# Performance work log

Hardware: AMD Instinct MI355X
Metric: run time of the kernel (lower is better)

The kernel has to match this reference:

```python
import jax, jax.numpy as jnp
import numpy as np
from jax import lax

H = 64
IN = 3

def _lstm_layer(x, Wih, Whh, bih, bhh, collect):
    # x: [B, T, in]; Wih: [4H, in]; Whh: [4H, H]. PyTorch gate order: i, f, g, o.
    B = x.shape[0]
    h0 = jnp.zeros((B, H), x.dtype)
    c0 = jnp.zeros((B, H), x.dtype)
    b = bih + bhh
    def step(carry, xt):
        h, c = carry
        gates = xt @ Wih.T + h @ Whh.T + b  # [B, 4H]
        i, f, g, o = jnp.split(gates, 4, axis=-1)
        i = jax.nn.sigmoid(i); f = jax.nn.sigmoid(f)
        g = jnp.tanh(g); o = jax.nn.sigmoid(o)
        c = f * c + i * g
        h = o * jnp.tanh(c)
        return (h, c), (h if collect else None)
    xs = jnp.swapaxes(x, 0, 1)  # [T, B, in]
    (h, c), hs = lax.scan(step, (h0, c0), xs)
    if collect:
        return jnp.swapaxes(hs, 0, 1)  # [B, T, H]
    return h  # [B, H]


def setup_inputs() -> dict:
    key = jax.random.key(0)
    ks = jax.random.split(key, 14)
    s = 1.0 / np.sqrt(H)
    def u(k, shape):
        return jax.random.uniform(k, shape, jnp.float32, -s, s)
    return {
        "x": jax.random.normal(ks[0], (4096, 512, IN), jnp.float32),
        "Wih0": u(ks[1], (4 * H, IN)), "Whh0": u(ks[2], (4 * H, H)),
        "bih0": u(ks[3], (4 * H,)), "bhh0": u(ks[4], (4 * H,)),
        "Wih1": u(ks[5], (4 * H, H)), "Whh1": u(ks[6], (4 * H, H)),
        "bih1": u(ks[7], (4 * H,)), "bhh1": u(ks[8], (4 * H,)),
        "Wc1": jax.random.normal(ks[9], (32, H), jnp.float32) * 0.1,
        "bc1": jnp.zeros((32,), jnp.float32),
        "Wc2": jax.random.normal(ks[10], (1, 32), jnp.float32) * 0.1,
        "bc2": jnp.zeros((1,), jnp.float32),
    }


def reference(x, Wih0, Whh0, bih0, bhh0, Wih1, Whh1, bih1, bhh1, Wc1, bc1, Wc2, bc2):
    # 2-layer LSTM (dropout inactive at inference); only last timestep of layer 2 is used.
    h1 = _lstm_layer(x, Wih0, Whh0, bih0, bhh0, collect=True)   # [B, T, H]
    last = _lstm_layer(h1, Wih1, Whh1, bih1, bhh1, collect=False)  # [B, H]
    hidden = jax.nn.relu(last @ Wc1.T + bc1)  # [B, 32]
    out = jax.nn.sigmoid(hidden @ Wc2.T + bc2)  # [B, 1]
    return out
```

## Files before the change

### kernel.cpp

```cpp
#include <hip/hip_runtime.h>

#define TSEQ   512
#define BATCH  4096
#define MROWS  16

typedef short bf16x8 __attribute__((ext_vector_type(8)));
typedef short bf16x4 __attribute__((ext_vector_type(4)));
typedef float f32x4  __attribute__((ext_vector_type(4)));
typedef float f32x2  __attribute__((ext_vector_type(2)));

#define NL2E  (-1.44269504f)
#define P2L2E (2.88539008f)

__device__ __forceinline__ unsigned short f2bf(float f) {
    unsigned int u = __builtin_bit_cast(unsigned int, f);
    return (unsigned short)((u + 0x8000u) >> 16);
}

__device__ __forceinline__ f32x2 cellupd2(const f32x4 a, const f32x4 b, f32x2& C) {
    f32x2 ei = {__builtin_amdgcn_exp2f(a[0]), __builtin_amdgcn_exp2f(b[0])};
    f32x2 ef = {__builtin_amdgcn_exp2f(a[1]), __builtin_amdgcn_exp2f(b[1])};
    f32x2 eg = {__builtin_amdgcn_exp2f(a[2]), __builtin_amdgcn_exp2f(b[2])};
    f32x2 eo = {__builtin_amdgcn_exp2f(a[3]), __builtin_amdgcn_exp2f(b[3])};
    f32x2 A  = 1.f + ei;
    f32x2 G1 = eg + 1.f;
    f32x2 F  = 1.f + ef;
    f32x2 t  = A * G1;
    f32x2 G2 = eg * P2L2E + (NL2E * 2.f);
    f32x2 num = C * t + G2 * F;
    f32x2 den = t * F;
    f32x2 r  = {__builtin_amdgcn_rcpf(den.x), __builtin_amdgcn_rcpf(den.y)};
    f32x2 Cn = num * r;
    Cn.x = fminf(Cn.x, 126.f);
    Cn.y = fminf(Cn.y, 126.f);
    C = Cn;
    f32x2 ec = {__builtin_amdgcn_exp2f(Cn.x), __builtin_amdgcn_exp2f(Cn.y)};
    f32x2 B  = 1.f + eo;
    f32x2 hn = ec - 1.f;
    f32x2 hd = B * (ec + 1.f);
    f32x2 rr = {__builtin_amdgcn_rcpf(hd.x), __builtin_amdgcn_rcpf(hd.y)};
    return hn * rr;
}


__global__ __launch_bounds__(1024, 4) void lstm2_kernel(
    const float* __restrict__ x,
    const float* __restrict__ Wih0, const float* __restrict__ Whh0,
    const float* __restrict__ bih0, const float* __restrict__ bhh0,
    const float* __restrict__ Wih1, const float* __restrict__ Whh1,
    const float* __restrict__ bih1, const float* __restrict__ bhh1,
    const float* __restrict__ Wc1,  const float* __restrict__ bc1,
    const float* __restrict__ Wc2,  const float* __restrict__ bc2,
    float* __restrict__ out)
{
    __shared__ __align__(16) unsigned short ring[2][MROWS * 64];
    __shared__ __align__(16) unsigned short h2s[2][MROWS * 64];
    __shared__ __align__(16) unsigned short xq[64][128];
    __shared__ float h2f[MROWS][65];
    __shared__ float hid[MROWS][33];

    const int tid  = threadIdx.x;
    const int wv   = tid >> 6;
    const int lane = tid & 63;
    const int col  = lane & 15;
    const int lg   = lane >> 4;
    const int b0   = blockIdx.x * MROWS;
    const int sw   = (col & 7) << 4;

    ((unsigned int*)ring)[tid] = 0u;
    ((unsigned int*)h2s)[tid]  = 0u;

    const int xrow = (tid >> 5) & 15;
    const int xt   = tid & 31;
    const float* xb = x + ((size_t)(b0 + xrow) * TSEQ + xt) * 3;
    float xr0 = 0.f, xr1 = 0.f, xr2 = 0.f;
    if (tid < 512) {
        xr0 = xb[0]; xr1 = xb[1]; xr2 = xb[2];
        bf16x8 xf = {(short)f2bf(xr0),(short)f2bf(xr1),(short)f2bf(xr2),0,0,0,0,0};
        *(bf16x8*)((char*)xq + (xt << 8) + ((xrow << 4) ^ ((xt & 7) << 4))) = xf;
        xr0 = xb[96]; xr1 = xb[97]; xr2 = xb[98];
    }
    __syncthreads();

    const int rd0 = (col * 128 +      lg * 16) ^ sw;
    const int rd1 = (col * 128 + 64 + lg * 16) ^ sw;

#define FLUSH(S) do { \
    if (((S) & 31) == 16 && (S) < 480) { \
        const int c1_ = ((S) >> 5) + 1; \
        const int t64_ = ((c1_ & 1) << 5) + xt; \
        bf16x8 xf_ = {(short)f2bf(xr0),(short)f2bf(xr1),(short)f2bf(xr2),0,0,0,0,0}; \
        *(bf16x8*)((char*)xq + (t64_ << 8) + ((xrow << 4) ^ ((xt & 7) << 4))) = xf_; \
        if (c1_ < 15) { const float* p_ = xb + (c1_ + 1) * 96; xr0 = p_[0]; xr1 = p_[1]; xr2 = p_[2]; } \
    } \
} while(0)

    if (wv < 8) {
        const int wq = wv;
        const int ga = col & 3;
        const float sca = (ga == 2) ? P2L2E : NL2E;
        bf16x8 Wf[2][3];
        f32x4 bia4[2];
#pragma unroll
        for (int tt = 0; tt < 2; ++tt) {
            const int n = ga * 64 + 16 * (col >> 2) + 2 * wq + tt;
#pragma unroll
            for (int f = 0; f < 3; ++f)
#pragma unroll
                for (int i = 0; i < 8; ++i) {
                    const int k = f * 32 + lg * 8 + i;
                    float v = 0.f;
                    if (k < 64)      v = Whh0[n * 64 + k];
                    else if (k < 67) v = Wih0[n * 3 + (k - 64)];
                    Wf[tt][f][i] = (short)f2bf(sca * v);
                }
#pragma unroll
            for (int r = 0; r < 4; ++r) {
                const int nb = r * 64 + 16 * lg + 2 * wq + tt;
                bia4[tt][r] = ((r == 2) ? P2L2E : NL2E) * (bih0[nb] + bhh0[nb]);
            }
        }
        const int hw = (col * 128 + 32 * lg + 4 * wq) ^ sw;
        f32x2 C01 = {0.f, 0.f};

#define L1B(RI, WI, S) do { \
        const char* rb_ = (const char*)ring[RI]; \
        bf16x8 v0_ = *(const bf16x8*)(rb_ + rd0); \
        bf16x8 v1_ = *(const bf16x8*)(rb_ + rd1); \
        bf16x8 v2_ = {0,0,0,0,0,0,0,0}; \
        if (lg == 0) \
            v2_ = *(const bf16x8*)((const char*)xq + ((((S)&63)) << 8) + ((col << 4) ^ (((S)&7) << 4))); \
        f32x4 a0_ = __builtin_amdgcn_mfma_f32_16x16x32_bf16(Wf[0][0], v0_, bia4[0],0,0,0); \
        f32x4 a1_ = __builtin_amdgcn_mfma_f32_16x16x32_bf16(Wf[1][0], v0_, bia4[1],0,0,0); \
        a0_ = __builtin_amdgcn_mfma_f32_16x16x32_bf16(Wf[0][1], v1_, a0_,0,0,0); \
        a1_ = __builtin_amdgcn_mfma_f32_16x16x32_bf16(Wf[1][1], v1_, a1_,0,0,0); \
        a0_ = __builtin_amdgcn_mfma_f32_16x16x32_bf16(Wf[0][2], v2_, a0_,0,0,0); \
        a1_ = __builtin_amdgcn_mfma_f32_16x16x32_bf16(Wf[1][2], v2_, a1_,0,0,0); \
        f32x2 h01_ = cellupd2(a0_, a1_, C01); \
        unsigned int p0_; \
        asm("v_cvt_pk_bf16_f32 %0, %1, %2" : "=v"(p0_) : "v"(h01_.x), "v"(h01_.y)); \
        *(unsigned int*)((char*)ring[WI] + hw) = p0_; \
    } while(0)

        L1B(1, 0, 0);
        __syncthreads();
#pragma unroll 1
        for (int m = 0; m < 255; ++m) {
            const int s1 = 2 * m + 1;
            L1B(0, 1, s1);
            __syncthreads();
            L1B(1, 0, s1 + 1);
            FLUSH(s1 + 1);
            __syncthreads();
        }
        L1B(0, 1, 511);
        __syncthreads();
        __syncthreads();
#undef L1B
    } else {
        const int wq = wv - 8;
        const int ga = col & 3;
        const float sca = (ga == 2) ? P2L2E : NL2E;
        bf16x8 Wf[2][4];
        f32x4 bia4[2];
#pragma unroll
        for (int tt = 0; tt < 2; ++tt) {
            const int n = ga * 64 + 16 * (col >> 2) + 2 * wq + tt;
#pragma unroll
            for (int f = 0; f < 4; ++f)
#pragma unroll
                for (int i = 0; i < 8; ++i) {
                    const int k = f * 32 + lg * 8 + i;
                    const float v = (k < 64) ? Wih1[n * 64 + k] : Whh1[n * 64 + (k - 64)];
                    Wf[tt][f][i] = (short)f2bf(sca * v);
                }
#pragma unroll
            for (int r = 0; r < 4; ++r) {
                const int nb = r * 64 + 16 * lg + 2 * wq + tt;
                bia4[tt][r] = ((r == 2) ? P2L2E : NL2E) * (bih1[nb] + bhh1[nb]);
            }
        }
        const int hw2 = (col * 128 + 32 * lg + 4 * wq) ^ sw;
        f32x2 C01 = {0.f, 0.f};
        f32x2 hv01 = {0.f, 0.f};

#define L2B(RB, HR) do { \
        const char* rb_ = (const char*)ring[RB]; \
        const char* hp_ = (const char*)h2s[HR]; \
        bf16x8 v0_ = *(const bf16x8*)(rb_ + rd0); \
        bf16x8 v1_ = *(const bf16x8*)(rb_ + rd1); \
        bf16x8 v2_ = *(const bf16x8*)(hp_ + rd0); \
        bf16x8 v3_ = *(const bf16x8*)(hp_ + rd1); \
        f32x4 a0_ = __builtin_amdgcn_mfma_f32_16x16x32_bf16(Wf[0][0], v0_, bia4[0],0,0,0); \
        f32x4 a1_ = __builtin_amdgcn_mfma_f32_16x16x32_bf16(Wf[1][0], v0_, bia4[1],0,0,0); \
        a0_ = __builtin_amdgcn_mfma_f32_16x16x32_bf16(Wf[0][1], v1_, a0_,0,0,0); \
        a1_ = __builtin_amdgcn_mfma_f32_16x16x32_bf16(Wf[1][1], v1_, a1_,0,0,0); \
        a0_ = __builtin_amdgcn_mfma_f32_16x16x32_bf16(Wf[0][2], v2_, a0_,0,0,0); \
        a1_ = __builtin_amdgcn_mfma_f32_16x16x32_bf16(Wf[1][2], v2_, a1_,0,0,0); \
        a0_ = __builtin_amdgcn_mfma_f32_16x16x32_bf16(Wf[0][3], v3_, a0_,0,0,0); \
        a1_ = __builtin_amdgcn_mfma_f32_16x16x32_bf16(Wf[1][3], v3_, a1_,0,0,0); \
        hv01 = cellupd2(a0_, a1_, C01); \
        unsigned int p0_; \
        asm("v_cvt_pk_bf16_f32 %0, %1, %2" : "=v"(p0_) : "v"(hv01.x), "v"(hv01.y)); \
        *(unsigned int*)((char*)h2s[RB] + hw2) = p0_; \
    } while(0)

        __syncthreads();
#pragma unroll 1
        for (int m = 0; m < 255; ++m) {
            L2B(0, 1);
            __syncthreads();
            L2B(1, 0);
            __syncthreads();
        }
        L2B(0, 1);
        __syncthreads();
        L2B(1, 0);
        __syncthreads();
#undef L2B
        const int ub = 16 * lg + 2 * wq;
        h2f[col][ub + 0] = hv01.x;
        h2f[col][ub + 1] = hv01.y;
    }
    __syncthreads();

    if (tid < 512) {
        const int b = tid & 15, j = tid >> 4;
        float s = bc1[j];
#pragma unroll 8
        for (int k = 0; k < 64; ++k) s += Wc1[j * 64 + k] * h2f[b][k];
        hid[b][j] = fmaxf(s, 0.f);
    }
    __syncthreads();
    if (tid < 16) {
        float s = bc2[0];
#pragma unroll 8
        for (int k = 0; k < 32; ++k) s += Wc2[k] * hid[tid][k];
        float e = __builtin_amdgcn_exp2f(NL2E * s);
        out[b0 + tid] = __builtin_amdgcn_rcpf(1.f + e);
    }
}

extern "C" void kernel_launch(void* const* d_in, const int* in_sizes, int n_in,
                              void* d_out, int out_size, void* d_ws, size_t ws_size,
                              hipStream_t stream) {
    lstm2_kernel<<<BATCH / MROWS, 1024, 0, stream>>>(
        (const float*)d_in[0],
        (const float*)d_in[1], (const float*)d_in[2],
        (const float*)d_in[3], (const float*)d_in[4],
        (const float*)d_in[5], (const float*)d_in[6],
        (const float*)d_in[7], (const float*)d_in[8],
        (const float*)d_in[9], (const float*)d_in[10],
        (const float*)d_in[11], (const float*)d_in[12],
        (float*)d_out);
}
```

Measured before the change: 293.3 us.

## Software-pipeline LDS operand loads across LSTM layer barriers with one-step lag

```diff
diff --git a/kernel.cpp b/kernel.cpp
--- a/kernel.cpp
+++ b/kernel.cpp
@@ -5,7 +5,6 @@
 #define MROWS  16
 
 typedef short bf16x8 __attribute__((ext_vector_type(8)));
-typedef short bf16x4 __attribute__((ext_vector_type(4)));
 typedef float f32x4  __attribute__((ext_vector_type(4)));
 typedef float f32x2  __attribute__((ext_vector_type(2)));
 
@@ -95,6 +94,8 @@
     } \
 } while(0)
 
+#define XQRD(S) (*(const bf16x8*)((const char*)xq + ((((S)&63)) << 8) + ((col << 4) ^ (((S)&7) << 4))))
+
     if (wv < 8) {
         const int wq = wv;
         const int ga = col & 3;
@@ -122,20 +123,19 @@
         }
         const int hw = (col * 128 + 32 * lg + 4 * wq) ^ sw;
         f32x2 C01 = {0.f, 0.f};
+        bf16x8 pv2 = XQRD(0);
 
 #define L1B(RI, WI, S) do { \
         const char* rb_ = (const char*)ring[RI]; \
         bf16x8 v0_ = *(const bf16x8*)(rb_ + rd0); \
         bf16x8 v1_ = *(const bf16x8*)(rb_ + rd1); \
-        bf16x8 v2_ = {0,0,0,0,0,0,0,0}; \
-        if (lg == 0) \
-            v2_ = *(const bf16x8*)((const char*)xq + ((((S)&63)) << 8) + ((col << 4) ^ (((S)&7) << 4))); \
-        f32x4 a0_ = __builtin_amdgcn_mfma_f32_16x16x32_bf16(Wf[0][0], v0_, bia4[0],0,0,0); \
-        f32x4 a1_ = __builtin_amdgcn_mfma_f32_16x16x32_bf16(Wf[1][0], v0_, bia4[1],0,0,0); \
+        f32x4 a0_ = __builtin_amdgcn_mfma_f32_16x16x32_bf16(Wf[0][2], pv2, bia4[0],0,0,0); \
+        f32x4 a1_ = __builtin_amdgcn_mfma_f32_16x16x32_bf16(Wf[1][2], pv2, bia4[1],0,0,0); \
+        a0_ = __builtin_amdgcn_mfma_f32_16x16x32_bf16(Wf[0][0], v0_, a0_,0,0,0); \
+        a1_ = __builtin_amdgcn_mfma_f32_16x16x32_bf16(Wf[1][0], v0_, a1_,0,0,0); \
         a0_ = __builtin_amdgcn_mfma_f32_16x16x32_bf16(Wf[0][1], v1_, a0_,0,0,0); \
         a1_ = __builtin_amdgcn_mfma_f32_16x16x32_bf16(Wf[1][1], v1_, a1_,0,0,0); \
-        a0_ = __builtin_amdgcn_mfma_f32_16x16x32_bf16(Wf[0][2], v2_, a0_,0,0,0); \
-        a1_ = __builtin_amdgcn_mfma_f32_16x16x32_bf16(Wf[1][2], v2_, a1_,0,0,0); \
+        pv2 = XQRD((S) + 1); \
         f32x2 h01_ = cellupd2(a0_, a1_, C01); \
         unsigned int p0_; \
         asm("v_cvt_pk_bf16_f32 %0, %1, %2" : "=v"(p0_) : "v"(h01_.x), "v"(h01_.y)); \
@@ -149,11 +149,12 @@
             const int s1 = 2 * m + 1;
             L1B(0, 1, s1);
             __syncthreads();
+            FLUSH(s1 + 1);
             L1B(1, 0, s1 + 1);
-            FLUSH(s1 + 1);
             __syncthreads();
         }
         L1B(0, 1, 511);
+        __syncthreads();
         __syncthreads();
         __syncthreads();
 #undef L1B
@@ -183,18 +184,23 @@
         const int hw2 = (col * 128 + 32 * lg + 4 * wq) ^ sw;
         f32x2 C01 = {0.f, 0.f};
         f32x2 hv01 = {0.f, 0.f};
-
-#define L2B(RB, HR) do { \
-        const char* rb_ = (const char*)ring[RB]; \
-        const char* hp_ = (const char*)h2s[HR]; \
-        bf16x8 v0_ = *(const bf16x8*)(rb_ + rd0); \
-        bf16x8 v1_ = *(const bf16x8*)(rb_ + rd1); \
+        bf16x8 pv0, pv1;
+
+#define PF(P) do { \
+        const char* pb_ = (const char*)ring[P]; \
+        pv0 = *(const bf16x8*)(pb_ + rd0); \
+        pv1 = *(const bf16x8*)(pb_ + rd1); \
+    } while(0)
+
+#define L2B(WB, PFC) do { \
+        const char* hp_ = (const char*)h2s[(WB) ^ 1]; \
         bf16x8 v2_ = *(const bf16x8*)(hp_ + rd0); \
         bf16x8 v3_ = *(const bf16x8*)(hp_ + rd1); \
-        f32x4 a0_ = __builtin_amdgcn_mfma_f32_16x16x32_bf16(Wf[0][0], v0_, bia4[0],0,0,0); \
-        f32x4 a1_ = __builtin_amdgcn_mfma_f32_16x16x32_bf16(Wf[1][0], v0_, bia4[1],0,0,0); \
-        a0_ = __builtin_amdgcn_mfma_f32_16x16x32_bf16(Wf[0][1], v1_, a0_,0,0,0); \
-        a1_ = __builtin_amdgcn_mfma_f32_16x16x32_bf16(Wf[1][1], v1_, a1_,0,0,0); \
+        f32x4 a0_ = __builtin_amdgcn_mfma_f32_16x16x32_bf16(Wf[0][0], pv0, bia4[0],0,0,0); \
+        f32x4 a1_ = __builtin_amdgcn_mfma_f32_16x16x32_bf16(Wf[1][0], pv0, bia4[1],0,0,0); \
+        a0_ = __builtin_amdgcn_mfma_f32_16x16x32_bf16(Wf[0][1], pv1, a0_,0,0,0); \
+        a1_ = __builtin_amdgcn_mfma_f32_16x16x32_bf16(Wf[1][1], pv1, a1_,0,0,0); \
+        PFC; \
         a0_ = __builtin_amdgcn_mfma_f32_16x16x32_bf16(Wf[0][2], v2_, a0_,0,0,0); \
         a1_ = __builtin_amdgcn_mfma_f32_16x16x32_bf16(Wf[1][2], v2_, a1_,0,0,0); \
         a0_ = __builtin_amdgcn_mfma_f32_16x16x32_bf16(Wf[0][3], v3_, a0_,0,0,0); \
@@ -202,22 +208,25 @@
         hv01 = cellupd2(a0_, a1_, C01); \
         unsigned int p0_; \
         asm("v_cvt_pk_bf16_f32 %0, %1, %2" : "=v"(p0_) : "v"(hv01.x), "v"(hv01.y)); \
-        *(unsigned int*)((char*)h2s[RB] + hw2) = p0_; \
+        *(unsigned int*)((char*)h2s[WB] + hw2) = p0_; \
     } while(0)
 
+        __syncthreads();
+        PF(0);
         __syncthreads();
 #pragma unroll 1
         for (int m = 0; m < 255; ++m) {
-            L2B(0, 1);
-            __syncthreads();
-            L2B(1, 0);
-            __syncthreads();
-        }
-        L2B(0, 1);
-        __syncthreads();
-        L2B(1, 0);
+            L2B(0, PF(1));
+            __syncthreads();
+            L2B(1, PF(0));
+            __syncthreads();
+        }
+        L2B(0, PF(1));
+        __syncthreads();
+        L2B(1, (void)0);
         __syncthreads();
 #undef L2B
+#undef PF
         const int ub = 16 * lg + 2 * wq;
         h2f[col][ub + 0] = hv01.x;
         h2f[col][ub + 1] = hv01.y;
```

New measurement: 299.4 us. +2.1%, slower.

## Merge both LSTM layers into each wave, halving block size

Applied to the files above, without the earlier changes.

```diff
diff --git a/kernel.cpp b/kernel.cpp
--- a/kernel.cpp
+++ b/kernel.cpp
@@ -5,7 +5,6 @@
 #define MROWS  16
 
 typedef short bf16x8 __attribute__((ext_vector_type(8)));
-typedef short bf16x4 __attribute__((ext_vector_type(4)));
 typedef float f32x4  __attribute__((ext_vector_type(4)));
 typedef float f32x2  __attribute__((ext_vector_type(2)));
 
@@ -43,7 +42,7 @@
 }
 
 
-__global__ __launch_bounds__(1024, 4) void lstm2_kernel(
+__global__ __launch_bounds__(512, 2) void lstm2_kernel(
     const float* __restrict__ x,
     const float* __restrict__ Wih0, const float* __restrict__ Whh0,
     const float* __restrict__ bih0, const float* __restrict__ bhh0,
@@ -67,19 +66,20 @@
     const int b0   = blockIdx.x * MROWS;
     const int sw   = (col & 7) << 4;
 
-    ((unsigned int*)ring)[tid] = 0u;
-    ((unsigned int*)h2s)[tid]  = 0u;
-
-    const int xrow = (tid >> 5) & 15;
+    for (int i = tid; i < 1024; i += 512) {
+        ((unsigned int*)ring)[i] = 0u;
+        ((unsigned int*)h2s)[i]  = 0u;
+    }
+
+    const int xrow = tid >> 5;
     const int xt   = tid & 31;
     const float* xb = x + ((size_t)(b0 + xrow) * TSEQ + xt) * 3;
-    float xr0 = 0.f, xr1 = 0.f, xr2 = 0.f;
-    if (tid < 512) {
-        xr0 = xb[0]; xr1 = xb[1]; xr2 = xb[2];
+    float xr0 = xb[0], xr1 = xb[1], xr2 = xb[2];
+    {
         bf16x8 xf = {(short)f2bf(xr0),(short)f2bf(xr1),(short)f2bf(xr2),0,0,0,0,0};
         *(bf16x8*)((char*)xq + (xt << 8) + ((xrow << 4) ^ ((xt & 7) << 4))) = xf;
-        xr0 = xb[96]; xr1 = xb[97]; xr2 = xb[98];
-    }
+    }
+    xr0 = xb[96]; xr1 = xb[97]; xr2 = xb[98];
     __syncthreads();
 
     const int rd0 = (col * 128 +      lg * 16) ^ sw;
@@ -95,136 +95,142 @@
     } \
 } while(0)
 
-    if (wv < 8) {
-        const int wq = wv;
-        const int ga = col & 3;
-        const float sca = (ga == 2) ? P2L2E : NL2E;
-        bf16x8 Wf[2][3];
-        f32x4 bia4[2];
-#pragma unroll
-        for (int tt = 0; tt < 2; ++tt) {
-            const int n = ga * 64 + 16 * (col >> 2) + 2 * wq + tt;
-#pragma unroll
-            for (int f = 0; f < 3; ++f)
-#pragma unroll
-                for (int i = 0; i < 8; ++i) {
-                    const int k = f * 32 + lg * 8 + i;
-                    float v = 0.f;
-                    if (k < 64)      v = Whh0[n * 64 + k];
-                    else if (k < 67) v = Wih0[n * 3 + (k - 64)];
-                    Wf[tt][f][i] = (short)f2bf(sca * v);
-                }
-#pragma unroll
-            for (int r = 0; r < 4; ++r) {
-                const int nb = r * 64 + 16 * lg + 2 * wq + tt;
-                bia4[tt][r] = ((r == 2) ? P2L2E : NL2E) * (bih0[nb] + bhh0[nb]);
+#define XQRD(S) (*(const bf16x8*)((const char*)xq + ((((S)&63)) << 8) + ((col << 4) ^ (((S)&7) << 4))))
+#define MM(A,B,C) __builtin_amdgcn_mfma_f32_16x16x32_bf16((A),(B),(C),0,0,0)
+
+    const int wq = wv;
+    const int ga = col & 3;
+    const float sca = (ga == 2) ? P2L2E : NL2E;
+    bf16x8 WfL1[2][3];
+    f32x4 biaL1[2];
+#pragma unroll
+    for (int tt = 0; tt < 2; ++tt) {
+        const int n = ga * 64 + 16 * (col >> 2) + 2 * wq + tt;
+#pragma unroll
+        for (int f = 0; f < 3; ++f)
+#pragma unroll
+            for (int i = 0; i < 8; ++i) {
+                const int k = f * 32 + lg * 8 + i;
+                float v = 0.f;
+                if (k < 64)      v = Whh0[n * 64 + k];
+                else if (k < 67) v = Wih0[n * 3 + (k - 64)];
+                WfL1[tt][f][i] = (short)f2bf(sca * v);
             }
+#pragma unroll
+        for (int r = 0; r < 4; ++r) {
+            const int nb = r * 64 + 16 * lg + 2 * wq + tt;
+            biaL1[tt][r] = ((r == 2) ? P2L2E : NL2E) * (bih0[nb] + bhh0[nb]);
         }
-        const int hw = (col * 128 + 32 * lg + 4 * wq) ^ sw;
-        f32x2 C01 = {0.f, 0.f};
-
-#define L1B(RI, WI, S) do { \
-        const char* rb_ = (const char*)ring[RI]; \
-        bf16x8 v0_ = *(const bf16x8*)(rb_ + rd0); \
-        bf16x8 v1_ = *(const bf16x8*)(rb_ + rd1); \
-        bf16x8 v2_ = {0,0,0,0,0,0,0,0}; \
-        if (lg == 0) \
-            v2_ = *(const bf16x8*)((const char*)xq + ((((S)&63)) << 8) + ((col << 4) ^ (((S)&7) << 4))); \
-        f32x4 a0_ = __builtin_amdgcn_mfma_f32_16x16x32_bf16(Wf[0][0], v0_, bia4[0],0,0,0); \
-        f32x4 a1_ = __builtin_amdgcn_mfma_f32_16x16x32_bf16(Wf[1][0], v0_, bia4[1],0,0,0); \
-        a0_ = __builtin_amdgcn_mfma_f32_16x16x32_bf16(Wf[0][1], v1_, a0_,0,0,0); \
-        a1_ = __builtin_amdgcn_mfma_f32_16x16x32_bf16(Wf[1][1], v1_, a1_,0,0,0); \
-        a0_ = __builtin_amdgcn_mfma_f32_16x16x32_bf16(Wf[0][2], v2_, a0_,0,0,0); \
-        a1_ = __builtin_amdgcn_mfma_f32_16x16x32_bf16(Wf[1][2], v2_, a1_,0,0,0); \
-        f32x2 h01_ = cellupd2(a0_, a1_, C01); \
-        unsigned int p0_; \
-        asm("v_cvt_pk_bf16_f32 %0, %1, %2" : "=v"(p0_) : "v"(h01_.x), "v"(h01_.y)); \
-        *(unsigned int*)((char*)ring[WI] + hw) = p0_; \
-    } while(0)
-
-        L1B(1, 0, 0);
-        __syncthreads();
-#pragma unroll 1
-        for (int m = 0; m < 255; ++m) {
-            const int s1 = 2 * m + 1;
-            L1B(0, 1, s1);
-            __syncthreads();
-            L1B(1, 0, s1 + 1);
-            FLUSH(s1 + 1);
-            __syncthreads();
+    }
+    bf16x8 WfL2[2][4];
+    f32x4 biaL2[2];
+#pragma unroll
+    for (int tt = 0; tt < 2; ++tt) {
+        const int n = ga * 64 + 16 * (col >> 2) + 2 * wq + tt;
+#pragma unroll
+        for (int f = 0; f < 4; ++f)
+#pragma unroll
+            for (int i = 0; i < 8; ++i) {
+                const int k = f * 32 + lg * 8 + i;
+                const float v = (k < 64) ? Wih1[n * 64 + k] : Whh1[n * 64 + (k - 64)];
+                WfL2[tt][f][i] = (short)f2bf(sca * v);
+            }
+#pragma unroll
+        for (int r = 0; r < 4; ++r) {
+            const int nb = r * 64 + 16 * lg + 2 * wq + tt;
+            biaL2[tt][r] = ((r == 2) ? P2L2E : NL2E) * (bih1[nb] + bhh1[nb]);
         }
-        L1B(0, 1, 511);
-        __syncthreads();
-        __syncthreads();
-#undef L1B
-    } else {
-        const int wq = wv - 8;
-        const int ga = col & 3;
-        const float sca = (ga == 2) ? P2L2E : NL2E;
-        bf16x8 Wf[2][4];
-        f32x4 bia4[2];
-#pragma unroll
-        for (int tt = 0; tt < 2; ++tt) {
-            const int n = ga * 64 + 16 * (col >> 2) + 2 * wq + tt;
-#pragma unroll
-            for (int f = 0; f < 4; ++f)
-#pragma unroll
-                for (int i = 0; i < 8; ++i) {
-                    const int k = f * 32 + lg * 8 + i;
-                    const float v = (k < 64) ? Wih1[n * 64 + k] : Whh1[n * 64 + (k - 64)];
-                    Wf[tt][f][i] = (short)f2bf(sca * v);
-                }
-#pragma unroll
-            for (int r = 0; r < 4; ++r) {
-                const int nb = r * 64 + 16 * lg + 2 * wq + tt;
-                bia4[tt][r] = ((r == 2) ? P2L2E : NL2E) * (bih1[nb] + bhh1[nb]);
-            }
-        }
-        const int hw2 = (col * 128 + 32 * lg + 4 * wq) ^ sw;
-        f32x2 C01 = {0.f, 0.f};
-        f32x2 hv01 = {0.f, 0.f};
-
-#define L2B(RB, HR) do { \
-        const char* rb_ = (const char*)ring[RB]; \
-        const char* hp_ = (const char*)h2s[HR]; \
+    }
+    const int hw = (col * 128 + 32 * lg + 4 * wq) ^ sw;
+    f32x2 C_L1 = {0.f, 0.f};
+    f32x2 C_L2 = {0.f, 0.f};
+    f32x2 hv01 = {0.f, 0.f};
+    bf16x8 pv2 = XQRD(0);
+
+#define MRG(P, S) do { \
+        const char* rb_ = (const char*)ring[P]; \
+        const char* hp_ = (const char*)h2s[(P) ^ 1]; \
         bf16x8 v0_ = *(const bf16x8*)(rb_ + rd0); \
         bf16x8 v1_ = *(const bf16x8*)(rb_ + rd1); \
         bf16x8 v2_ = *(const bf16x8*)(hp_ + rd0); \
         bf16x8 v3_ = *(const bf16x8*)(hp_ + rd1); \
-        f32x4 a0_ = __builtin_amdgcn_mfma_f32_16x16x32_bf16(Wf[0][0], v0_, bia4[0],0,0,0); \
-        f32x4 a1_ = __builtin_amdgcn_mfma_f32_16x16x32_bf16(Wf[1][0], v0_, bia4[1],0,0,0); \
-        a0_ = __builtin_amdgcn_mfma_f32_16x16x32_bf16(Wf[0][1], v1_, a0_,0,0,0); \
-        a1_ = __builtin_amdgcn_mfma_f32_16x16x32_bf16(Wf[1][1], v1_, a1_,0,0,0); \
-        a0_ = __builtin_amdgcn_mfma_f32_16x16x32_bf16(Wf[0][2], v2_, a0_,0,0,0); \
-        a1_ = __builtin_amdgcn_mfma_f32_16x16x32_bf16(Wf[1][2], v2_, a1_,0,0,0); \
-        a0_ = __builtin_amdgcn_mfma_f32_16x16x32_bf16(Wf[0][3], v3_, a0_,0,0,0); \
-        a1_ = __builtin_amdgcn_mfma_f32_16x16x32_bf16(Wf[1][3], v3_, a1_,0,0,0); \
-        hv01 = cellupd2(a0_, a1_, C01); \
+        f32x4 b0_ = MM(WfL1[0][2], pv2, biaL1[0]); \
+        f32x4 b1_ = MM(WfL1[1][2], pv2, biaL1[1]); \
+        b0_ = MM(WfL1[0][0], v0_, b0_); \
+        b1_ = MM(WfL1[1][0], v0_, b1_); \
+        f32x4 c0_ = MM(WfL2[0][0], v0_, biaL2[0]); \
+        f32x4 c1_ = MM(WfL2[1][0], v0_, biaL2[1]); \
+        b0_ = MM(WfL1[0][1], v1_, b0_); \
+        b1_ = MM(WfL1[1][1], v1_, b1_); \
+        pv2 = XQRD((S) + 1); \
+        f32x2 hL1_ = cellupd2(b0_, b1_, C_L1); \
+        c0_ = MM(WfL2[0][1], v1_, c0_); \
+        c1_ = MM(WfL2[1][1], v1_, c1_); \
+        c0_ = MM(WfL2[0][2], v2_, c0_); \
+        c1_ = MM(WfL2[1][2], v2_, c1_); \
+        c0_ = MM(WfL2[0][3], v3_, c0_); \
+        c1_ = MM(WfL2[1][3], v3_, c1_); \
         unsigned int p0_; \
-        asm("v_cvt_pk_bf16_f32 %0, %1, %2" : "=v"(p0_) : "v"(hv01.x), "v"(hv01.y)); \
-        *(unsigned int*)((char*)h2s[RB] + hw2) = p0_; \
+        asm("v_cvt_pk_bf16_f32 %0, %1, %2" : "=v"(p0_) : "v"(hL1_.x), "v"(hL1_.y)); \
+        *(unsigned int*)((char*)ring[(P) ^ 1] + hw) = p0_; \
+        hv01 = cellupd2(c0_, c1_, C_L2); \
+        unsigned int p1_; \
+        asm("v_cvt_pk_bf16_f32 %0, %1, %2" : "=v"(p1_) : "v"(hv01.x), "v"(hv01.y)); \
+        *(unsigned int*)((char*)h2s[P] + hw) = p1_; \
     } while(0)
 
+    {
+        const char* rb_ = (const char*)ring[1];
+        bf16x8 v0_ = *(const bf16x8*)(rb_ + rd0);
+        bf16x8 v1_ = *(const bf16x8*)(rb_ + rd1);
+        f32x4 b0_ = MM(WfL1[0][2], pv2, biaL1[0]);
+        f32x4 b1_ = MM(WfL1[1][2], pv2, biaL1[1]);
+        b0_ = MM(WfL1[0][0], v0_, b0_);
+        b1_ = MM(WfL1[1][0], v0_, b1_);
+        b0_ = MM(WfL1[0][1], v1_, b0_);
+        b1_ = MM(WfL1[1][1], v1_, b1_);
+        pv2 = XQRD(1);
+        f32x2 hL1_ = cellupd2(b0_, b1_, C_L1);
+        unsigned int p0_;
+        asm("v_cvt_pk_bf16_f32 %0, %1, %2" : "=v"(p0_) : "v"(hL1_.x), "v"(hL1_.y));
+        *(unsigned int*)((char*)ring[0] + hw) = p0_;
+    }
+    __syncthreads();
+
+#pragma unroll 1
+    for (int m = 0; m < 255; ++m) {
+        MRG(0, 2 * m + 1);
         __syncthreads();
-#pragma unroll 1
-        for (int m = 0; m < 255; ++m) {
-            L2B(0, 1);
-            __syncthreads();
-            L2B(1, 0);
-            __syncthreads();
-        }
-        L2B(0, 1);
+        FLUSH(2 * m + 2);
+        MRG(1, 2 * m + 2);
         __syncthreads();
-        L2B(1, 0);
-        __syncthreads();
-#undef L2B
-        const int ub = 16 * lg + 2 * wq;
-        h2f[col][ub + 0] = hv01.x;
-        h2f[col][ub + 1] = hv01.y;
-    }
-    __syncthreads();
-
-    if (tid < 512) {
+    }
+    MRG(0, 511);
+    __syncthreads();
+
+    {
+        const char* rb_ = (const char*)ring[1];
+        const char* hp_ = (const char*)h2s[0];
+        bf16x8 v0_ = *(const bf16x8*)(rb_ + rd0);
+        bf16x8 v1_ = *(const bf16x8*)(rb_ + rd1);
+        bf16x8 v2_ = *(const bf16x8*)(hp_ + rd0);
+        bf16x8 v3_ = *(const bf16x8*)(hp_ + rd1);
+        f32x4 c0_ = MM(WfL2[0][0], v0_, biaL2[0]);
+        f32x4 c1_ = MM(WfL2[1][0], v0_, biaL2[1]);
+        c0_ = MM(WfL2[0][1], v1_, c0_);
+        c1_ = MM(WfL2[1][1], v1_, c1_);
+        c0_ = MM(WfL2[0][2], v2_, c0_);
+        c1_ = MM(WfL2[1][2], v2_, c1_);
+        c0_ = MM(WfL2[0][3], v3_, c0_);
+        c1_ = MM(WfL2[1][3], v3_, c1_);
+        hv01 = cellupd2(c0_, c1_, C_L2);
+    }
+    const int ub = 16 * lg + 2 * wq;
+    h2f[col][ub + 0] = hv01.x;
+    h2f[col][ub + 1] = hv01.y;
+    __syncthreads();
+
+    {
         const int b = tid & 15, j = tid >> 4;
         float s = bc1[j];
 #pragma unroll 8
@@ -244,7 +250,7 @@
 extern "C" void kernel_launch(void* const* d_in, const int* in_sizes, int n_in,
                               void* d_out, int out_size, void* d_ws, size_t ws_size,
                               hipStream_t stream) {
-    lstm2_kernel<<<BATCH / MROWS, 1024, 0, stream>>>(
+    lstm2_kernel<<<BATCH / MROWS, 512, 0, stream>>>(
         (const float*)d_in[0],
         (const float*)d_in[1], (const float*)d_in[2],
         (const float*)d_in[3], (const float*)d_in[4],
```

New measurement: 326.4 us. 11.3% more time.

## Halve batch rows per block, use 512-thread blocks with swizzled MFMA outputs

Applied to the files above, without the earlier changes.

```diff
diff --git a/kernel.cpp b/kernel.cpp
--- a/kernel.cpp
+++ b/kernel.cpp
@@ -2,10 +2,9 @@
 
 #define TSEQ   512
 #define BATCH  4096
-#define MROWS  16
+#define MROWS  8
 
 typedef short bf16x8 __attribute__((ext_vector_type(8)));
-typedef short bf16x4 __attribute__((ext_vector_type(4)));
 typedef float f32x4  __attribute__((ext_vector_type(4)));
 typedef float f32x2  __attribute__((ext_vector_type(2)));
 
@@ -42,8 +41,17 @@
     return hn * rr;
 }
 
-
-__global__ __launch_bounds__(1024, 4) void lstm2_kernel(
+__device__ __forceinline__ f32x4 swz8(f32x4 v) {
+    f32x4 r;
+#pragma unroll
+    for (int i = 0; i < 4; ++i)
+        r[i] = __builtin_bit_cast(float,
+                 __builtin_amdgcn_ds_swizzle(__builtin_bit_cast(int, v[i]), 0x201F));
+    return r;
+}
+
+
+__global__ __launch_bounds__(512, 4) void lstm2_kernel(
     const float* __restrict__ x,
     const float* __restrict__ Wih0, const float* __restrict__ Whh0,
     const float* __restrict__ bih0, const float* __restrict__ bhh0,
@@ -53,9 +61,9 @@
     const float* __restrict__ Wc2,  const float* __restrict__ bc2,
     float* __restrict__ out)
 {
-    __shared__ __align__(16) unsigned short ring[2][MROWS * 64];
-    __shared__ __align__(16) unsigned short h2s[2][MROWS * 64];
-    __shared__ __align__(16) unsigned short xq[64][128];
+    __shared__ __align__(16) unsigned short ring[2][16 * 64];
+    __shared__ __align__(16) unsigned short h2s[2][16 * 64];
+    __shared__ __align__(16) unsigned short xq[64][64];
     __shared__ float h2f[MROWS][65];
     __shared__ float hid[MROWS][33];
 
@@ -66,44 +74,67 @@
     const int lg   = lane >> 4;
     const int b0   = blockIdx.x * MROWS;
     const int sw   = (col & 7) << 4;
-
-    ((unsigned int*)ring)[tid] = 0u;
-    ((unsigned int*)h2s)[tid]  = 0u;
-
-    const int xrow = (tid >> 5) & 15;
+    const int colr = col & 7;
+    const int tsel = col >> 3;
+    const bool hi  = (col & 8) != 0;
+
+    for (int i = tid; i < 1024; i += 512) {
+        ((unsigned int*)ring)[i] = 0u;
+        ((unsigned int*)h2s)[i]  = 0u;
+    }
+
+    const int xrow = (tid >> 5) & 7;
     const int xt   = tid & 31;
     const float* xb = x + ((size_t)(b0 + xrow) * TSEQ + xt) * 3;
     float xr0 = 0.f, xr1 = 0.f, xr2 = 0.f;
-    if (tid < 512) {
+    if (tid < 256) {
         xr0 = xb[0]; xr1 = xb[1]; xr2 = xb[2];
         bf16x8 xf = {(short)f2bf(xr0),(short)f2bf(xr1),(short)f2bf(xr2),0,0,0,0,0};
-        *(bf16x8*)((char*)xq + (xt << 8) + ((xrow << 4) ^ ((xt & 7) << 4))) = xf;
+        *(bf16x8*)((char*)xq + (xt << 7) + ((xrow << 4) ^ ((xt & 7) << 4))) = xf;
         xr0 = xb[96]; xr1 = xb[97]; xr2 = xb[98];
     }
     __syncthreads();
 
     const int rd0 = (col * 128 +      lg * 16) ^ sw;
     const int rd1 = (col * 128 + 64 + lg * 16) ^ sw;
+    const int hwr = (colr * 128 + 32 * lg + 8 * (wv & 3) + 4 * tsel) ^ (colr << 4);
 
 #define FLUSH(S) do { \
     if (((S) & 31) == 16 && (S) < 480) { \
         const int c1_ = ((S) >> 5) + 1; \
         const int t64_ = ((c1_ & 1) << 5) + xt; \
         bf16x8 xf_ = {(short)f2bf(xr0),(short)f2bf(xr1),(short)f2bf(xr2),0,0,0,0,0}; \
-        *(bf16x8*)((char*)xq + (t64_ << 8) + ((xrow << 4) ^ ((xt & 7) << 4))) = xf_; \
+        *(bf16x8*)((char*)xq + (t64_ << 7) + ((xrow << 4) ^ ((xt & 7) << 4))) = xf_; \
         if (c1_ < 15) { const float* p_ = xb + (c1_ + 1) * 96; xr0 = p_[0]; xr1 = p_[1]; xr2 = p_[2]; } \
     } \
 } while(0)
 
-    if (wv < 8) {
+#define XQRD(S) (*(const bf16x8*)((const char*)xq + ((((S)&63)) << 7) + ((colr << 4) ^ (((S)&7) << 4))))
+#define MM(A,B,C) __builtin_amdgcn_mfma_f32_16x16x32_bf16((A),(B),(C),0,0,0)
+
+#define FINISH(A0,A1,A2,A3, CST, BUFBASE) do { \
+        f32x4 s2_ = swz8(A2), s3_ = swz8(A3); \
+        f32x4 sa_, sb_; \
+        _Pragma("unroll") \
+        for (int i_ = 0; i_ < 4; ++i_) { \
+            sa_[i_] = hi ? s2_[i_] : A0[i_]; \
+            sb_[i_] = hi ? s3_[i_] : A1[i_]; \
+        } \
+        hcur = cellupd2(sa_, sb_, CST); \
+        unsigned int p0_; \
+        asm("v_cvt_pk_bf16_f32 %0, %1, %2" : "=v"(p0_) : "v"(hcur.x), "v"(hcur.y)); \
+        *(unsigned int*)((char*)(BUFBASE) + hwr) = p0_; \
+    } while(0)
+
+    if (wv < 4) {
         const int wq = wv;
         const int ga = col & 3;
         const float sca = (ga == 2) ? P2L2E : NL2E;
-        bf16x8 Wf[2][3];
-        f32x4 bia4[2];
-#pragma unroll
-        for (int tt = 0; tt < 2; ++tt) {
-            const int n = ga * 64 + 16 * (col >> 2) + 2 * wq + tt;
+        bf16x8 Wf[4][3];
+        f32x4 bia4[4];
+#pragma unroll
+        for (int tt = 0; tt < 4; ++tt) {
+            const int n = ga * 64 + 16 * (col >> 2) + 4 * wq + tt;
 #pragma unroll
             for (int f = 0; f < 3; ++f)
 #pragma unroll
@@ -116,30 +147,28 @@
                 }
 #pragma unroll
             for (int r = 0; r < 4; ++r) {
-                const int nb = r * 64 + 16 * lg + 2 * wq + tt;
+                const int nb = r * 64 + 16 * lg + 4 * wq + tt;
                 bia4[tt][r] = ((r == 2) ? P2L2E : NL2E) * (bih0[nb] + bhh0[nb]);
             }
         }
-        const int hw = (col * 128 + 32 * lg + 4 * wq) ^ sw;
         f32x2 C01 = {0.f, 0.f};
+        f32x2 hcur;
+        bf16x8 pv2 = XQRD(0);
 
 #define L1B(RI, WI, S) do { \
         const char* rb_ = (const char*)ring[RI]; \
         bf16x8 v0_ = *(const bf16x8*)(rb_ + rd0); \
         bf16x8 v1_ = *(const bf16x8*)(rb_ + rd1); \
-        bf16x8 v2_ = {0,0,0,0,0,0,0,0}; \
-        if (lg == 0) \
-            v2_ = *(const bf16x8*)((const char*)xq + ((((S)&63)) << 8) + ((col << 4) ^ (((S)&7) << 4))); \
-        f32x4 a0_ = __builtin_amdgcn_mfma_f32_16x16x32_bf16(Wf[0][0], v0_, bia4[0],0,0,0); \
-        f32x4 a1_ = __builtin_amdgcn_mfma_f32_16x16x32_bf16(Wf[1][0], v0_, bia4[1],0,0,0); \
-        a0_ = __builtin_amdgcn_mfma_f32_16x16x32_bf16(Wf[0][1], v1_, a0_,0,0,0); \
-        a1_ = __builtin_amdgcn_mfma_f32_16x16x32_bf16(Wf[1][1], v1_, a1_,0,0,0); \
-        a0_ = __builtin_amdgcn_mfma_f32_16x16x32_bf16(Wf[0][2], v2_, a0_,0,0,0); \
-        a1_ = __builtin_amdgcn_mfma_f32_16x16x32_bf16(Wf[1][2], v2_, a1_,0,0,0); \
-        f32x2 h01_ = cellupd2(a0_, a1_, C01); \
-        unsigned int p0_; \
-        asm("v_cvt_pk_bf16_f32 %0, %1, %2" : "=v"(p0_) : "v"(h01_.x), "v"(h01_.y)); \
-        *(unsigned int*)((char*)ring[WI] + hw) = p0_; \
+        f32x4 a0_ = MM(Wf[0][2], pv2, bia4[0]); \
+        f32x4 a1_ = MM(Wf[1][2], pv2, bia4[1]); \
+        f32x4 a2_ = MM(Wf[2][2], pv2, bia4[2]); \
+        f32x4 a3_ = MM(Wf[3][2], pv2, bia4[3]); \
+        a0_ = MM(Wf[0][0], v0_, a0_);  a1_ = MM(Wf[1][0], v0_, a1_); \
+        a2_ = MM(Wf[2][0], v0_, a2_);  a3_ = MM(Wf[3][0], v0_, a3_); \
+        a0_ = MM(Wf[0][1], v1_, a0_);  a1_ = MM(Wf[1][1], v1_, a1_); \
+        a2_ = MM(Wf[2][1], v1_, a2_);  a3_ = MM(Wf[3][1], v1_, a3_); \
+        pv2 = XQRD((S) + 1); \
+        FINISH(a0_, a1_, a2_, a3_, C01, ring[WI]); \
     } while(0)
 
         L1B(1, 0, 0);
@@ -158,14 +187,14 @@
         __syncthreads();
 #undef L1B
     } else {
-        const int wq = wv - 8;
+        const int wq = wv - 4;
         const int ga = col & 3;
         const float sca = (ga == 2) ? P2L2E : NL2E;
-        bf16x8 Wf[2][4];
-        f32x4 bia4[2];
-#pragma unroll
-        for (int tt = 0; tt < 2; ++tt) {
-            const int n = ga * 64 + 16 * (col >> 2) + 2 * wq + tt;
+        bf16x8 Wf[4][4];
+        f32x4 bia4[4];
+#pragma unroll
+        for (int tt = 0; tt < 4; ++tt) {
+            const int n = ga * 64 + 16 * (col >> 2) + 4 * wq + tt;
 #pragma unroll
             for (int f = 0; f < 4; ++f)
 #pragma unroll
@@ -176,13 +205,12 @@
                 }
 #pragma unroll
             for (int r = 0; r < 4; ++r) {
-                const int nb = r * 64 + 16 * lg + 2 * wq + tt;
+                const int nb = r * 64 + 16 * lg + 4 * wq + tt;
                 bia4[tt][r] = ((r == 2) ? P2L2E : NL2E) * (bih1[nb] + bhh1[nb]);
             }
         }
-        const int hw2 = (col * 128 + 32 * lg + 4 * wq) ^ sw;
         f32x2 C01 = {0.f, 0.f};
-        f32x2 hv01 = {0.f, 0.f};
+        f32x2 hcur = {0.f, 0.f};
 
 #define L2B(RB, HR) do { \
         const char* rb_ = (const char*)ring[RB]; \
@@ -191,18 +219,17 @@
         bf16x8 v1_ = *(const bf16x8*)(rb_ + rd1); \
         bf16x8 v2_ = *(const bf16x8*)(hp_ + rd0); \
         bf16x8 v3_ = *(const bf16x8*)(hp_ + rd1); \
-        f32x4 a0_ = __builtin_amdgcn_mfma_f32_16x16x32_bf16(Wf[0][0], v0_, bia4[0],0,0,0); \
-        f32x4 a1_ = __builtin_amdgcn_mfma_f32_16x16x32_bf16(Wf[1][0], v0_, bia4[1],0,0,0); \
-        a0_ = __builtin_amdgcn_mfma_f32_16x16x32_bf16(Wf[0][1], v1_, a0_,0,0,0); \
-        a1_ = __builtin_amdgcn_mfma_f32_16x16x32_bf16(Wf[1][1], v1_, a1_,0,0,0); \
-        a0_ = __builtin_amdgcn_mfma_f32_16x16x32_bf16(Wf[0][2], v2_, a0_,0,0,0); \
-        a1_ = __builtin_amdgcn_mfma_f32_16x16x32_bf16(Wf[1][2], v2_, a1_,0,0,0); \
-        a0_ = __builtin_amdgcn_mfma_f32_16x16x32_bf16(Wf[0][3], v3_, a0_,0,0,0); \
-        a1_ = __builtin_amdgcn_mfma_f32_16x16x32_bf16(Wf[1][3], v3_, a1_,0,0,0); \
-        hv01 = cellupd2(a0_, a1_, C01); \
-        unsigned int p0_; \
-        asm("v_cvt_pk_bf16_f32 %0, %1, %2" : "=v"(p0_) : "v"(hv01.x), "v"(hv01.y)); \
-        *(unsigned int*)((char*)h2s[RB] + hw2) = p0_; \
+        f32x4 c0_ = MM(Wf[0][0], v0_, bia4[0]); \
+        f32x4 c1_ = MM(Wf[1][0], v0_, bia4[1]); \
+        f32x4 c2_ = MM(Wf[2][0], v0_, bia4[2]); \
+        f32x4 c3_ = MM(Wf[3][0], v0_, bia4[3]); \
+        c0_ = MM(Wf[0][1], v1_, c0_);  c1_ = MM(Wf[1][1], v1_, c1_); \
+        c2_ = MM(Wf[2][1], v1_, c2_);  c3_ = MM(Wf[3][1], v1_, c3_); \
+        c0_ = MM(Wf[0][2], v2_, c0_);  c1_ = MM(Wf[1][2], v2_, c1_); \
+        c2_ = MM(Wf[2][2], v2_, c2_);  c3_ = MM(Wf[3][2], v2_, c3_); \
+        c0_ = MM(Wf[0][3], v3_, c0_);  c1_ = MM(Wf[1][3], v3_, c1_); \
+        c2_ = MM(Wf[2][3], v3_, c2_);  c3_ = MM(Wf[3][3], v3_, c3_); \
+        FINISH(c0_, c1_, c2_, c3_, C01, h2s[RB]); \
     } while(0)
 
         __syncthreads();
@@ -218,21 +245,21 @@
         L2B(1, 0);
         __syncthreads();
 #undef L2B
-        const int ub = 16 * lg + 2 * wq;
-        h2f[col][ub + 0] = hv01.x;
-        h2f[col][ub + 1] = hv01.y;
+        const int ub = 16 * lg + 4 * wq + 2 * tsel;
+        h2f[colr][ub + 0] = hcur.x;
+        h2f[colr][ub + 1] = hcur.y;
     }
     __syncthreads();
 
-    if (tid < 512) {
-        const int b = tid & 15, j = tid >> 4;
+    if (tid < 256) {
+        const int b = tid & 7, j = tid >> 3;
         float s = bc1[j];
 #pragma unroll 8
         for (int k = 0; k < 64; ++k) s += Wc1[j * 64 + k] * h2f[b][k];
         hid[b][j] = fmaxf(s, 0.f);
     }
     __syncthreads();
-    if (tid < 16) {
+    if (tid < MROWS) {
         float s = bc2[0];
 #pragma unroll 8
         for (int k = 0; k < 32; ++k) s += Wc2[k] * hid[tid][k];
@@ -244,7 +271,7 @@
 extern "C" void kernel_launch(void* const* d_in, const int* in_sizes, int n_in,
                               void* d_out, int out_size, void* d_ws, size_t ws_size,
                               hipStream_t stream) {
-    lstm2_kernel<<<BATCH / MROWS, 1024, 0, stream>>>(
+    lstm2_kernel<<<BATCH / MROWS, 512, 0, stream>>>(
         (const float*)d_in[0],
         (const float*)d_in[1], (const float*)d_in[2],
         (const float*)d_in[3], (const float*)d_in[4],
```

Result: slower. 412.3 us (+40.5%).
